# Kernel tuning notes

Measured on AMD Instinct MI355X. Metric: run time of the kernel, lower is better.

## Reference

```python
import jax, jax.numpy as jnp
import numpy as np

DROP_I = 0.75  # input dropout prob
DROP_S = 0.25  # state dropout prob
DEPTH = 3      # recur_depth
NOISE_SEED = 42


def setup_inputs() -> dict:
    key = jax.random.key(0)
    ks = jax.random.split(key, 8)
    B, T, Din, D = 32, 2048, 512, 512
    s = 0.04  # init_scale
    u = lambda k, shape: jax.random.uniform(k, shape, jnp.float32, -s, s)
    return {
        "h0": jnp.zeros((1, D), jnp.float32),
        "seq": jax.random.normal(ks[0], (B, T, Din), jnp.float32),
        "wH": u(ks[1], (Din, D)),
        "bH": u(ks[2], (D,)),
        "wT": u(ks[3], (Din, D)),
        "bT": jnp.full((D,), -2.0, jnp.float32),  # init_T_bias
        "recurH_w": u(ks[4], (DEPTH, D, D)),
        # layer 0 has no bias in the source -> zero row is equivalent math
        "recurH_b": jnp.concatenate([jnp.zeros((1, D), jnp.float32), u(ks[5], (DEPTH - 1, D))], 0),
        "recurT_w": u(ks[6], (DEPTH, D, D)),
        "recurT_b": jnp.concatenate([jnp.zeros((1, D), jnp.float32), jnp.full((DEPTH - 1, D), -2.0, jnp.float32)], 0),
    }


def _dropout_noise(key, p_drop, shape, dtype):
    keep = 1.0 - p_drop
    return jax.random.bernoulli(key, keep, shape).astype(dtype) / keep


def _forward(h0, seq, wH, bH, wT, bT, recurH_w, recurH_b, recurT_w, recurT_b):
    B, T, Din = seq.shape
    D = wH.shape[1]
    k1, k2 = jax.random.split(jax.random.key(NOISE_SEED))
    # tied_noise=True: one input-noise mask shared by H/T paths, one state-noise mask
    noise_i = _dropout_noise(k1, DROP_I, (B, Din), seq.dtype)  # [B, Din], shared over time
    noise_s = _dropout_noise(k2, DROP_S, (B, D), seq.dtype)    # [B, D], shared over time & depth

    x = seq * noise_i[:, None, :]                              # [B, T, Din]
    i_H = jnp.einsum('btd,de->bte', x, wH) + bH                # [B, T, D]
    i_T = jnp.einsum('btd,de->bte', x, wT) + bT

    # Faithful to source: every timestep starts from H0 (state is not carried),
    # so time is a parallel axis and only the depth loop is sequential.
    s = jnp.broadcast_to(h0.reshape(1, 1, D), (B, T, D))
    for l in range(DEPTH):
        sd = s * noise_s[:, None, :]
        h_lin = jnp.einsum('btd,de->bte', sd, recurH_w[l]) + recurH_b[l]
        t_lin = jnp.einsum('btd,de->bte', sd, recurT_w[l]) + recurT_b[l]
        if l == 0:
            h_lin = h_lin + i_H
            t_lin = t_lin + i_T
        Hg = jnp.tanh(h_lin)
        Tg = jax.nn.sigmoid(t_lin)
        s = (Hg - s) * Tg + s  # highway combine
    return s  # [B, T, D]


def reference(h0, seq, wH, bH, wT, bT, recurH_w, recurH_b, recurT_w, recurT_b):
    return _forward(h0, seq, wH, bH, wT, bT, recurH_w, recurH_b, recurT_w, recurT_b)
```

## Files before the change

### kernel.cpp

```cpp
#include <hip/hip_runtime.h>
#include <stdint.h>
#include <math.h>

#define B_SZ   32
#define T_LEN  2048
#define DIN    512
#define DD     512
#define M_TOT  (B_SZ * T_LEN)
#define NTHREADS 256
#define WSZ    ((size_t)DD * DD)

typedef unsigned short u16;
typedef __attribute__((ext_vector_type(8))) short short8;
typedef __attribute__((ext_vector_type(4))) float f32x4;

__device__ __forceinline__ u16 f2bf(float f) {
  uint32_t u = __float_as_uint(f);
  uint32_t r = (u + 0x7FFFu + ((u >> 16) & 1u)) >> 16;
  return (u16)r;
}

typedef const void __attribute__((address_space(1)))* as1cp;
typedef void __attribute__((address_space(3)))* as3p;
__device__ __forceinline__ void async16(const void* g, void* l) {
  __builtin_amdgcn_global_load_lds((as1cp)(uintptr_t)g,
                                   (as3p)(uint32_t)(uintptr_t)l, 16, 0, 0);
}

__device__ __forceinline__ uint32_t rotl32(uint32_t x, int n) {
  return (x << n) | (x >> (32 - n));
}

__device__ __forceinline__ void threefry2x32(uint32_t k0, uint32_t k1,
                                             uint32_t x0, uint32_t x1,
                                             uint32_t& o0, uint32_t& o1) {
  const uint32_t ks0 = k0, ks1 = k1, ks2 = k0 ^ k1 ^ 0x1BD11BDAu;
  uint32_t v0 = x0 + ks0, v1 = x1 + ks1;
#define TF_R(r) { v0 += v1; v1 = rotl32(v1, (r)); v1 ^= v0; }
  TF_R(13) TF_R(15) TF_R(26) TF_R(6)
  v0 += ks1; v1 += ks2 + 1u;
  TF_R(17) TF_R(29) TF_R(16) TF_R(24)
  v0 += ks2; v1 += ks0 + 2u;
  TF_R(13) TF_R(15) TF_R(26) TF_R(6)
  v0 += ks0; v1 += ks1 + 3u;
  TF_R(17) TF_R(29) TF_R(16) TF_R(24)
  v0 += ks1; v1 += ks2 + 4u;
  TF_R(13) TF_R(15) TF_R(26) TF_R(6)
  v0 += ks2; v1 += ks0 + 5u;
#undef TF_R
  o0 = v0; o1 = v1;
}

__global__ void noise_kernel(float* __restrict__ noise_i, float* __restrict__ noise_s) {
  int i = blockIdx.x * blockDim.x + threadIdx.x;
  if (i >= B_SZ * DIN) return;
  uint32_t k1a, k1b, k2a, k2b;
  threefry2x32(0u, 42u, 0u, 0u, k1a, k1b);
  threefry2x32(0u, 42u, 0u, 1u, k2a, k2b);
  uint32_t b1, b2;
  threefry2x32(k1a, k1b, 0u, (uint32_t)i, b1, b2);
  noise_i[i] = (b1 < 0x40000000u) ? 4.0f : 0.0f;
  threefry2x32(k2a, k2b, 0u, (uint32_t)i, b1, b2);
  noise_s[i] = (b1 < 0xC0000000u) ? (1.0f / 0.75f) : 0.0f;
}

__global__ __launch_bounds__(256) void vec0_kernel(
    const float* __restrict__ h0, const float* __restrict__ noise_s,
    const float* __restrict__ rHw, const float* __restrict__ rHb,
    const float* __restrict__ rTw, const float* __restrict__ rTb,
    float* __restrict__ vH0, float* __restrict__ vT0) {
  __shared__ float sdv[DD];
  const int b = blockIdx.x >> 1;
  const int c = (blockIdx.x & 1) * 256 + threadIdx.x;
  for (int k = threadIdx.x; k < DD; k += 256)
    sdv[k] = h0[k] * noise_s[b * DD + k];
  __syncthreads();
  float aH = 0.f, aT = 0.f;
  for (int k = 0; k < DD; ++k) {
    float v = sdv[k];
    aH += v * rHw[(size_t)k * DD + c];
    aT += v * rTw[(size_t)k * DD + c];
  }
  vH0[b * DD + c] = aH + rHb[c];
  vT0[b * DD + c] = aT + rTb[c];
}

__global__ __launch_bounds__(256) void wt_all(
    const float* __restrict__ wH, const float* __restrict__ wT,
    const float* __restrict__ rHw, const float* __restrict__ rTw,
    u16* __restrict__ Wt) {
  __shared__ float tile[64][68];
  const int which = blockIdx.x >> 6;
  const float* W;
  switch (which) {
    case 0: W = wH; break;
    case 1: W = wT; break;
    case 2: W = rHw + WSZ; break;
    case 3: W = rTw + WSZ; break;
    case 4: W = rHw + 2 * WSZ; break;
    default: W = rTw + 2 * WSZ; break;
  }
  u16* dst = Wt + (size_t)which * WSZ;
  const int tb = blockIdx.x & 63;
  const int kt = (tb >> 3) * 64;
  const int nt = (tb & 7) * 64;
  const int tid = threadIdx.x;
  {
    int r = tid >> 2;
#pragma unroll
    for (int u = 0; u < 4; ++u) {
      int c = ((tid & 3) + u * 4) * 4;
      float4 v = *(const float4*)(W + (size_t)(kt + r) * DD + nt + c);
      tile[r][c] = v.x; tile[r][c + 1] = v.y; tile[r][c + 2] = v.z; tile[r][c + 3] = v.w;
    }
  }
  __syncthreads();
  {
    int n = tid >> 2, seg = (tid & 3) * 16;
    u16 o[16];
#pragma unroll
    for (int u = 0; u < 16; ++u) o[u] = f2bf(tile[seg + u][n]);
    *(uint4*)(dst + (size_t)(nt + n) * DD + kt + seg) = *(const uint4*)o;
    *(uint4*)(dst + (size_t)(nt + n) * DD + kt + seg + 8) = *(const uint4*)(o + 8);
  }
}

__global__ __launch_bounds__(256) void xprep(const float* __restrict__ seq,
                                             const float* __restrict__ noise_i,
                                             u16* __restrict__ Xbf) {
  int idx = blockIdx.x * 256 + threadIdx.x;
  int row = idx >> 6;
  int k8 = (idx & 63) * 8;
  int b = row >> 11;
  const float* s = seq + (size_t)row * DIN + k8;
  const float* n = noise_i + b * DIN + k8;
  float4 s0 = *(const float4*)s, s1 = *(const float4*)(s + 4);
  float4 n0 = *(const float4*)n, n1 = *(const float4*)(n + 4);
  u16 o[8];
  o[0] = f2bf(s0.x * n0.x); o[1] = f2bf(s0.y * n0.y);
  o[2] = f2bf(s0.z * n0.z); o[3] = f2bf(s0.w * n0.w);
  o[4] = f2bf(s1.x * n1.x); o[5] = f2bf(s1.y * n1.y);
  o[6] = f2bf(s1.z * n1.z); o[7] = f2bf(s1.w * n1.w);
  *(uint4*)(Xbf + (size_t)idx * 8) = *(const uint4*)o;
}

__global__ __launch_bounds__(256, 3) void layer_gemm(
    const u16* __restrict__ Abf,
    const u16* __restrict__ WtH,
    const u16* __restrict__ WtT,
    const float* __restrict__ hbv,
    const float* __restrict__ tbv,
    const float* __restrict__ vH0,
    const float* __restrict__ vT0,
    const float* __restrict__ h0,
    const float* __restrict__ noise_s,
    const float* Sprev,
    float* Snew,
    u16* __restrict__ SDnew,
    float* Out,
    int layer) {
  __shared__ u16 lds[20480];
  u16* ldsA  = lds;
  u16* ldsBH = lds + 4096;
  u16* ldsBT = lds + 12288;

  const int tid  = threadIdx.x;
  const int lane = tid & 63, wid = tid >> 6;
  const int bid  = (blockIdx.x & 7) * 512 + (blockIdx.x >> 3);
  const int m0   = (bid >> 2) * 64;
  const int c0   = (bid & 3) * 128;
  const int bidx = m0 >> 11;
  const int q  = lane >> 4, mr = lane & 15;
  const int wqm = wid >> 1, wqn = wid & 1;

  const u16* gA[2]; const u16* gBH[4]; const u16* gBT[4];
  u16* lA[2]; u16* lBH[4]; u16* lBT[4];
#pragma unroll
  for (int t = 0; t < 2; ++t) {
    int s  = tid + t * 256;
    int rm = s >> 3;
    int k8 = (s & 7) ^ (rm & 7);
    gA[t] = Abf + (size_t)(m0 + rm) * DD + k8 * 8;
    lA[t] = ldsA + s * 8;
  }
#pragma unroll
  for (int t = 0; t < 4; ++t) {
    int s  = tid + t * 256;
    int rm = s >> 3;
    int k8 = (s & 7) ^ (rm & 7);
    gBH[t] = WtH + (size_t)(c0 + rm) * DD + k8 * 8;
    gBT[t] = WtT + (size_t)(c0 + rm) * DD + k8 * 8;
    lBH[t] = ldsBH + s * 8;
    lBT[t] = ldsBT + s * 8;
  }

  f32x4 accH[2][4], accT[2][4];
#pragma unroll
  for (int i = 0; i < 2; ++i)
#pragma unroll
    for (int j = 0; j < 4; ++j) {
      accH[i][j] = (f32x4){0.f, 0.f, 0.f, 0.f};
      accT[i][j] = (f32x4){0.f, 0.f, 0.f, 0.f};
    }

  for (int kb = 0; kb < 8; ++kb) {
    __syncthreads();
    const int ko = kb * 64;
#pragma unroll
    for (int t = 0; t < 2; ++t) async16(gA[t] + ko, lA[t]);
#pragma unroll
    for (int t = 0; t < 4; ++t) {
      async16(gBH[t] + ko, lBH[t]);
      async16(gBT[t] + ko, lBT[t]);
    }
    __syncthreads();

#pragma unroll
    for (int ks = 0; ks < 2; ++ks) {
      const int jj = ((((ks << 2) + q) ^ (mr & 7)) << 3);
      short8 a[2];
#pragma unroll
      for (int mt = 0; mt < 2; ++mt)
        a[mt] = *(const short8*)(ldsA + (wqm * 32 + mt * 16 + mr) * 64 + jj);
#pragma unroll
      for (int nt = 0; nt < 4; ++nt) {
        int nofs = (wqn * 64 + nt * 16 + mr) * 64 + jj;
        short8 bh = *(const short8*)(ldsBH + nofs);
        short8 bt = *(const short8*)(ldsBT + nofs);
#pragma unroll
        for (int mt = 0; mt < 2; ++mt) {
          accH[mt][nt] = __builtin_amdgcn_mfma_f32_16x16x32_bf16(a[mt], bh, accH[mt][nt], 0, 0, 0);
          accT[mt][nt] = __builtin_amdgcn_mfma_f32_16x16x32_bf16(a[mt], bt, accT[mt][nt], 0, 0, 0);
        }
      }
    }
  }

  const int b512 = bidx * DD;
#pragma unroll
  for (int nt = 0; nt < 4; ++nt) {
    const int gc = c0 + wqn * 64 + nt * 16 + mr;
    float hb = hbv[gc], tb = tbv[gc];
    float nsc = 0.f, h0c = 0.f;
    if (layer == 0) {
      hb += vH0[b512 + gc];
      tb += vT0[b512 + gc];
      h0c = h0[gc];
    }
    if (layer < 2) nsc = noise_s[b512 + gc];
#pragma unroll
    for (int mt = 0; mt < 2; ++mt) {
      const int gmb = m0 + wqm * 32 + mt * 16 + q * 4;
#pragma unroll
      for (int r = 0; r < 4; ++r) {
        const size_t o = (size_t)(gmb + r) * DD + gc;
        float sp = (layer == 0) ? h0c : Sprev[o];
        float hg = tanhf(accH[mt][nt][r] + hb);
        float tg = 1.f / (1.f + __expf(-(accT[mt][nt][r] + tb)));
        float sn = (hg - sp) * tg + sp;
        if (layer < 2) {
          Snew[o] = sn;
          SDnew[o] = f2bf(sn * nsc);
        } else {
          Out[o] = sn;
        }
      }
    }
  }
}

extern "C" void kernel_launch(void* const* d_in, const int* in_sizes, int n_in,
                              void* d_out, int out_size, void* d_ws, size_t ws_size,
                              hipStream_t stream) {
  const float* h0  = (const float*)d_in[0];
  const float* seq = (const float*)d_in[1];
  const float* wH  = (const float*)d_in[2];
  const float* bH  = (const float*)d_in[3];
  const float* wT  = (const float*)d_in[4];
  const float* bT  = (const float*)d_in[5];
  const float* rHw = (const float*)d_in[6];
  const float* rHb = (const float*)d_in[7];
  const float* rTw = (const float*)d_in[8];
  const float* rTb = (const float*)d_in[9];
  float* out = (float*)d_out;

  char* ws = (char*)d_ws;
  float* noise_i = (float*)(ws);
  float* noise_s = (float*)(ws + (64 << 10));
  float* vH0     = (float*)(ws + (128 << 10));
  float* vT0     = (float*)(ws + (192 << 10));
  u16* Wt    = (u16*)(ws + (256 << 10));
  u16* Xbf   = (u16*)(ws + (4ull << 20));
  u16* SD0   = (u16*)(ws + (68ull << 20));

  noise_kernel<<<64, 256, 0, stream>>>(noise_i, noise_s);
  vec0_kernel<<<64, 256, 0, stream>>>(h0, noise_s, rHw, rHb, rTw, rTb, vH0, vT0);
  wt_all<<<384, 256, 0, stream>>>(wH, wT, rHw, rTw, Wt);
  xprep<<<M_TOT * DIN / 8 / 256, 256, 0, stream>>>(seq, noise_i, Xbf);

  const int NBLK = (M_TOT / 64) * (DD / 128);
  layer_gemm<<<NBLK, NTHREADS, 0, stream>>>(
      Xbf, Wt + 0 * WSZ, Wt + 1 * WSZ, bH, bT, vH0, vT0, h0, noise_s,
      nullptr, out, SD0, nullptr, 0);
  layer_gemm<<<NBLK, NTHREADS, 0, stream>>>(
      SD0, Wt + 2 * WSZ, Wt + 3 * WSZ, rHb + DD, rTb + DD, nullptr, nullptr, h0, noise_s,
      out, out, Xbf, nullptr, 1);
  layer_gemm<<<NBLK, NTHREADS, 0, stream>>>(
      Xbf, Wt + 4 * WSZ, Wt + 5 * WSZ, rHb + 2 * DD, rTb + 2 * DD, nullptr, nullptr, h0, noise_s,
      out, nullptr, nullptr, out, 2);
}
```

Before: 721.9 us.

## Fuse dropout scaling and bf16 conversion into GEMM A-tile loads

Drops the separate xprep pass and the per-layer bf16 dropped-state buffer. Each layer GEMM now reads the fp32 input or state directly, multiplies it by a dropout mask cached in LDS, and packs it to bf16 with v_cvt_pk_bf16_f32 before writing to LDS. This removes one full pass over seq and the extra bf16 state writes and reads. In exchange, A-tile traffic is fp32 (twice the bytes) through synchronous register loads instead of async global-to-LDS copies, and state ping-pongs between out and a workspace buffer.

```diff
diff --git a/kernel.cpp b/kernel.cpp
--- a/kernel.cpp
+++ b/kernel.cpp
@@ -13,11 +13,18 @@
 typedef unsigned short u16;
 typedef __attribute__((ext_vector_type(8))) short short8;
 typedef __attribute__((ext_vector_type(4))) float f32x4;
+typedef __attribute__((ext_vector_type(4))) unsigned int u32x4;
 
 __device__ __forceinline__ u16 f2bf(float f) {
   uint32_t u = __float_as_uint(f);
   uint32_t r = (u + 0x7FFFu + ((u >> 16) & 1u)) >> 16;
   return (u16)r;
+}
+
+__device__ __forceinline__ uint32_t cvtpk(float lo, float hi) {
+  uint32_t r;
+  asm("v_cvt_pk_bf16_f32 %0, %1, %2" : "=v"(r) : "v"(lo), "v"(hi));
+  return r;
 }
 
 typedef const void __attribute__((address_space(1)))* as1cp;
@@ -125,27 +132,9 @@
   }
 }
 
-__global__ __launch_bounds__(256) void xprep(const float* __restrict__ seq,
-                                             const float* __restrict__ noise_i,
-                                             u16* __restrict__ Xbf) {
-  int idx = blockIdx.x * 256 + threadIdx.x;
-  int row = idx >> 6;
-  int k8 = (idx & 63) * 8;
-  int b = row >> 11;
-  const float* s = seq + (size_t)row * DIN + k8;
-  const float* n = noise_i + b * DIN + k8;
-  float4 s0 = *(const float4*)s, s1 = *(const float4*)(s + 4);
-  float4 n0 = *(const float4*)n, n1 = *(const float4*)(n + 4);
-  u16 o[8];
-  o[0] = f2bf(s0.x * n0.x); o[1] = f2bf(s0.y * n0.y);
-  o[2] = f2bf(s0.z * n0.z); o[3] = f2bf(s0.w * n0.w);
-  o[4] = f2bf(s1.x * n1.x); o[5] = f2bf(s1.y * n1.y);
-  o[6] = f2bf(s1.z * n1.z); o[7] = f2bf(s1.w * n1.w);
-  *(uint4*)(Xbf + (size_t)idx * 8) = *(const uint4*)o;
-}
-
 __global__ __launch_bounds__(256, 3) void layer_gemm(
-    const u16* __restrict__ Abf,
+    const float* __restrict__ Asrc,
+    const float* __restrict__ nzv,
     const u16* __restrict__ WtH,
     const u16* __restrict__ WtT,
     const float* __restrict__ hbv,
@@ -153,13 +142,10 @@
     const float* __restrict__ vH0,
     const float* __restrict__ vT0,
     const float* __restrict__ h0,
-    const float* __restrict__ noise_s,
-    const float* Sprev,
-    float* Snew,
-    u16* __restrict__ SDnew,
-    float* Out,
+    float* __restrict__ Snew,
     int layer) {
   __shared__ u16 lds[20480];
+  __shared__ float nzl[DD];
   u16* ldsA  = lds;
   u16* ldsBH = lds + 4096;
   u16* ldsBT = lds + 12288;
@@ -173,16 +159,20 @@
   const int q  = lane >> 4, mr = lane & 15;
   const int wqm = wid >> 1, wqn = wid & 1;
 
-  const u16* gA[2]; const u16* gBH[4]; const u16* gBT[4];
-  u16* lA[2]; u16* lBH[4]; u16* lBT[4];
+  for (int k = tid; k < DD; k += 256) nzl[k] = nzv[bidx * DD + k];
+
+  const float* gAsrc[2]; u16* lAdst[2]; int nzofs[2];
 #pragma unroll
   for (int t = 0; t < 2; ++t) {
-    int s  = tid + t * 256;
-    int rm = s >> 3;
-    int k8 = (s & 7) ^ (rm & 7);
-    gA[t] = Abf + (size_t)(m0 + rm) * DD + k8 * 8;
-    lA[t] = ldsA + s * 8;
-  }
+    int s = tid + t * 256;
+    int row = s >> 3;
+    int k8 = (s & 7) ^ (row & 7);
+    gAsrc[t] = Asrc + (size_t)(m0 + row) * DD + k8 * 8;
+    lAdst[t] = ldsA + s * 8;
+    nzofs[t] = k8 * 8;
+  }
+  const u16* gBH[4]; const u16* gBT[4];
+  u16* lBH[4]; u16* lBT[4];
 #pragma unroll
   for (int t = 0; t < 4; ++t) {
     int s  = tid + t * 256;
@@ -206,12 +196,27 @@
   for (int kb = 0; kb < 8; ++kb) {
     __syncthreads();
     const int ko = kb * 64;
-#pragma unroll
-    for (int t = 0; t < 2; ++t) async16(gA[t] + ko, lA[t]);
+    float4 av0[2], av1[2];
+#pragma unroll
+    for (int t = 0; t < 2; ++t) {
+      av0[t] = *(const float4*)(gAsrc[t] + ko);
+      av1[t] = *(const float4*)(gAsrc[t] + ko + 4);
+    }
 #pragma unroll
     for (int t = 0; t < 4; ++t) {
       async16(gBH[t] + ko, lBH[t]);
       async16(gBT[t] + ko, lBT[t]);
+    }
+#pragma unroll
+    for (int t = 0; t < 2; ++t) {
+      const float4 n0 = *(const float4*)&nzl[ko + nzofs[t]];
+      const float4 n1 = *(const float4*)&nzl[ko + nzofs[t] + 4];
+      u32x4 pk;
+      pk.x = cvtpk(av0[t].x * n0.x, av0[t].y * n0.y);
+      pk.y = cvtpk(av0[t].z * n0.z, av0[t].w * n0.w);
+      pk.z = cvtpk(av1[t].x * n1.x, av1[t].y * n1.y);
+      pk.w = cvtpk(av1[t].z * n1.z, av1[t].w * n1.w);
+      *(u32x4*)lAdst[t] = pk;
     }
     __syncthreads();
 
@@ -241,29 +246,22 @@
   for (int nt = 0; nt < 4; ++nt) {
     const int gc = c0 + wqn * 64 + nt * 16 + mr;
     float hb = hbv[gc], tb = tbv[gc];
-    float nsc = 0.f, h0c = 0.f;
+    float h0c = 0.f;
     if (layer == 0) {
       hb += vH0[b512 + gc];
       tb += vT0[b512 + gc];
       h0c = h0[gc];
     }
-    if (layer < 2) nsc = noise_s[b512 + gc];
 #pragma unroll
     for (int mt = 0; mt < 2; ++mt) {
       const int gmb = m0 + wqm * 32 + mt * 16 + q * 4;
 #pragma unroll
       for (int r = 0; r < 4; ++r) {
         const size_t o = (size_t)(gmb + r) * DD + gc;
-        float sp = (layer == 0) ? h0c : Sprev[o];
+        float sp = (layer == 0) ? h0c : Asrc[o];
         float hg = tanhf(accH[mt][nt][r] + hb);
         float tg = 1.f / (1.f + __expf(-(accT[mt][nt][r] + tb)));
-        float sn = (hg - sp) * tg + sp;
-        if (layer < 2) {
-          Snew[o] = sn;
-          SDnew[o] = f2bf(sn * nsc);
-        } else {
-          Out[o] = sn;
-        }
+        Snew[o] = (hg - sp) * tg + sp;
       }
     }
   }
@@ -289,23 +287,21 @@
   float* noise_s = (float*)(ws + (64 << 10));
   float* vH0     = (float*)(ws + (128 << 10));
   float* vT0     = (float*)(ws + (192 << 10));
-  u16* Wt    = (u16*)(ws + (256 << 10));
-  u16* Xbf   = (u16*)(ws + (4ull << 20));
-  u16* SD0   = (u16*)(ws + (68ull << 20));
+  u16* Wt        = (u16*)(ws + (256 << 10));
+  float* Sbuf    = (float*)(ws + (4ull << 20));
 
   noise_kernel<<<64, 256, 0, stream>>>(noise_i, noise_s);
   vec0_kernel<<<64, 256, 0, stream>>>(h0, noise_s, rHw, rHb, rTw, rTb, vH0, vT0);
   wt_all<<<384, 256, 0, stream>>>(wH, wT, rHw, rTw, Wt);
-  xprep<<<M_TOT * DIN / 8 / 256, 256, 0, stream>>>(seq, noise_i, Xbf);
 
   const int NBLK = (M_TOT / 64) * (DD / 128);
   layer_gemm<<<NBLK, NTHREADS, 0, stream>>>(
-      Xbf, Wt + 0 * WSZ, Wt + 1 * WSZ, bH, bT, vH0, vT0, h0, noise_s,
-      nullptr, out, SD0, nullptr, 0);
+      seq, noise_i, Wt + 0 * WSZ, Wt + 1 * WSZ, bH, bT, vH0, vT0, h0,
+      out, 0);
   layer_gemm<<<NBLK, NTHREADS, 0, stream>>>(
-      SD0, Wt + 2 * WSZ, Wt + 3 * WSZ, rHb + DD, rTb + DD, nullptr, nullptr, h0, noise_s,
-      out, out, Xbf, nullptr, 1);
+      out, noise_s, Wt + 2 * WSZ, Wt + 3 * WSZ, rHb + DD, rTb + DD, vH0, vT0, h0,
+      Sbuf, 1);
   layer_gemm<<<NBLK, NTHREADS, 0, stream>>>(
-      Xbf, Wt + 4 * WSZ, Wt + 5 * WSZ, rHb + 2 * DD, rTb + 2 * DD, nullptr, nullptr, h0, noise_s,
-      out, nullptr, nullptr, out, 2);
-}
+      Sbuf, noise_s, Wt + 4 * WSZ, Wt + 5 * WSZ, rHb + 2 * DD, rTb + 2 * DD, vH0, vT0, h0,
+      out, 2);
+}
```

Measured after the change: 687.7 us. 1.05x faster.
